# Kernel optimization log

Measured on AMD Instinct MI355X. Metric: run time of the kernel, lower is better.

Reference implementation:

```python
import jax, jax.numpy as jnp
import numpy as np

N_NODES = 100000
N_EDGES = 1600000
D = 64
L = 4
D_TGT = 32


def setup_inputs() -> dict:
    key = jax.random.key(0)
    ks = jax.random.split(key, 8)
    x = jax.random.normal(ks[0], (N_NODES, D), dtype=jnp.float32)
    edge_index = jax.random.randint(ks[1], (2, N_EDGES), 0, N_NODES, dtype=jnp.int64)
    s = 1.0 / np.sqrt(D)
    Wl = jax.random.normal(ks[2], (L, D, D), dtype=jnp.float32) * s
    bl = jnp.zeros((L, D), dtype=jnp.float32)
    Wr = jax.random.normal(ks[3], (L, D, D), dtype=jnp.float32) * s
    Wp = jax.random.normal(ks[4], (L * D, D_TGT), dtype=jnp.float32) * (1.0 / np.sqrt(L * D))
    bp = jnp.zeros((D_TGT,), dtype=jnp.float32)
    return {"x": x, "edge_index": edge_index, "Wl": Wl, "bl": bl, "Wr": Wr, "Wp": Wp, "bp": bp}


def reference(x, edge_index, Wl, bl, Wr, Wp, bp):
    src, dst = edge_index[0], edge_index[1]
    n = x.shape[0]
    # in-degree per node, clamped to avoid div-by-zero (PyG mean gives 0 for isolated nodes;
    # sum is 0 there so clamping matches)
    deg = jax.ops.segment_sum(jnp.ones_like(dst, dtype=x.dtype), dst, num_segments=n)
    deg = jnp.maximum(deg, 1.0)[:, None]
    h = x
    outs = []
    for i in range(Wl.shape[0]):
        # SAGEConv: out = lin_l(mean_{j in N(i)} h_j) + lin_r(h_i)
        agg = jax.ops.segment_sum(h[src], dst, num_segments=n) / deg
        h = agg @ Wl[i] + bl[i] + h @ Wr[i]
        outs.append(h)
    h_cat = jnp.concatenate(outs, axis=1)  # [N, L*D]
    return h_cat @ Wp + bp  # [N, D_TGT]
```

## Files before the change

### kernel.cpp

```cpp
#include <hip/hip_runtime.h>
#include <hip/hip_fp16.h>

#define NN 100000
#define NE 1600000
#define NNP (NN + 64)

#define NPB 512
#define NBUK ((NN + NPB - 1) / NPB)
#define EPB 2048
#define ABLK ((NE + EPB - 1) / EPB)
#define BCAP 10240

typedef _Float16 half8 __attribute__((ext_vector_type(8)));
typedef float f32x4 __attribute__((ext_vector_type(4)));


__global__ __launch_bounds__(256) void bucket_init(int* __restrict__ bucket_cur) {
  int t = blockIdx.x * 256 + threadIdx.x;
  if (t < NBUK) bucket_cur[t] = t * BCAP;
}

__global__ __launch_bounds__(256) void binA(const int* __restrict__ src,
                                            const int* __restrict__ dst,
                                            int* __restrict__ bucket_cur,
                                            uint2* __restrict__ binned) {
  __shared__ int hist[NBUK];
  __shared__ int sc[256];
  __shared__ int lbase[NBUK];
  __shared__ int gbase[NBUK];
  __shared__ int lcur[NBUK];
  __shared__ uint2 stage[EPB];
  int t = threadIdx.x;
  int e0 = blockIdx.x * EPB;
  if (t < NBUK) hist[t] = 0;
  __syncthreads();
  int es[8], ed[8];
#pragma unroll
  for (int j = 0; j < 8; ++j) {
    int e = e0 + t + j * 256;
    if (e < NE) {
      es[j] = src[e];
      ed[j] = dst[e];
      atomicAdd(&hist[ed[j] >> 9], 1);
    } else {
      es[j] = -1;
      ed[j] = 0;
    }
  }
  __syncthreads();
  sc[t] = (t < NBUK) ? hist[t] : 0;
  __syncthreads();
  for (int off = 1; off < 256; off <<= 1) {
    int v = (t >= off) ? sc[t - off] : 0;
    __syncthreads();
    sc[t] += v;
    __syncthreads();
  }
  if (t < NBUK) {
    int h = hist[t];
    int lb = sc[t] - h;
    lbase[t] = lb;
    lcur[t] = lb;
    if (h > 0) gbase[t] = atomicAdd(&bucket_cur[t], h);
  }
  __syncthreads();
#pragma unroll
  for (int j = 0; j < 8; ++j) {
    if (es[j] >= 0) {
      int b = ed[j] >> 9;
      int slot = atomicAdd(&lcur[b], 1);
      stage[slot] = make_uint2((unsigned)es[j], (unsigned)ed[j]);
    }
  }
  __syncthreads();
  int total = min(EPB, NE - e0);
  for (int i = t; i < total; i += 256) {
    uint2 p = stage[i];
    int b = (int)(p.y >> 9);
    binned[(size_t)gbase[b] + (i - lbase[b])] = p;
  }
}

__global__ __launch_bounds__(256) void bucket_scan(const int* __restrict__ bucket_cur,
                                                   int* __restrict__ bucket_base,
                                                   int* __restrict__ row_ptr) {
  __shared__ int part[256];
  int t = threadIdx.x;
  int v = (t < NBUK) ? (bucket_cur[t] - t * BCAP) : 0;
  part[t] = v;
  __syncthreads();
  for (int off = 1; off < 256; off <<= 1) {
    int u = (t >= off) ? part[t - off] : 0;
    __syncthreads();
    part[t] += u;
    __syncthreads();
  }
  if (t < NBUK) bucket_base[t] = part[t] - v;
  if (t == 0) row_ptr[NN] = NE;
}

__global__ __launch_bounds__(256) void binB(const uint2* __restrict__ binned,
                                            const int* __restrict__ bucket_cur,
                                            const int* __restrict__ bucket_base,
                                            int* __restrict__ row_ptr,
                                            float* __restrict__ deg_inv,
                                            int* __restrict__ col) {
  __shared__ int hist[NPB];
  __shared__ int cur2[NPB];
  __shared__ int part[256];
  __shared__ int srcS[BCAP];
  int b = blockIdx.x;
  int n0 = b * NPB;
  int n1 = min(n0 + NPB, NN);
  int cnt = bucket_cur[b] - b * BCAP;
  int gb = bucket_base[b];
  size_t seg = (size_t)b * BCAP;
  int t = threadIdx.x;
  hist[t] = 0;
  hist[t + 256] = 0;
  __syncthreads();
  for (int i = t; i < cnt; i += 256)
    atomicAdd(&hist[(int)binned[seg + i].y - n0], 1);
  __syncthreads();
  int c0 = hist[2 * t], c1 = hist[2 * t + 1];
  int s = c0 + c1;
  part[t] = s;
  __syncthreads();
  for (int off = 1; off < 256; off <<= 1) {
    int u = (t >= off) ? part[t - off] : 0;
    __syncthreads();
    part[t] += u;
    __syncthreads();
  }
  int excl = part[t] - s;
  cur2[2 * t] = excl;
  cur2[2 * t + 1] = excl + c0;
  int n = n0 + 2 * t;
  if (n < n1) {
    row_ptr[n] = gb + excl;
    deg_inv[n] = 1.0f / (float)(c0 > 1 ? c0 : 1);
  }
  if (n + 1 < n1) {
    row_ptr[n + 1] = gb + excl + c0;
    deg_inv[n + 1] = 1.0f / (float)(c1 > 1 ? c1 : 1);
  }
  __syncthreads();
  for (int i = t; i < cnt; i += 256) {
    uint2 p = binned[seg + i];
    int slot = atomicAdd(&cur2[(int)p.y - n0], 1);
    srcS[slot] = (int)p.x;
  }
  __syncthreads();
  for (int i = t; i < cnt; i += 256) col[(size_t)gb + i] = srcS[i];
}


__global__ __launch_bounds__(256) void tohalf(const float* __restrict__ x,
                                              __half* __restrict__ x16) {
  size_t o = ((size_t)blockIdx.x * 256 + threadIdx.x) * 8;
  float4 a = *(const float4*)(x + o);
  float4 b = *(const float4*)(x + o + 4);
  union { uint4 u; __half h[8]; } U;
  U.h[0] = __float2half(a.x); U.h[1] = __float2half(a.y);
  U.h[2] = __float2half(a.z); U.h[3] = __float2half(a.w);
  U.h[4] = __float2half(b.x); U.h[5] = __float2half(b.y);
  U.h[6] = __float2half(b.z); U.h[7] = __float2half(b.w);
  *(uint4*)(x16 + o) = U.u;
}


__global__ __launch_bounds__(256) void prep_weights(const float* __restrict__ Wl,
                                                    const float* __restrict__ Wr,
                                                    const float* __restrict__ Wp,
                                                    _Float16* __restrict__ WcatT,
                                                    _Float16* __restrict__ WpT) {
  int t = blockIdx.x * 256 + threadIdx.x;
  if (t < 4 * 64 * 128) {
    int l = t >> 13, rem = t & 8191, j = rem >> 7, k = rem & 127;
    float v = (k < 64) ? Wl[l * 4096 + k * 64 + j] : Wr[l * 4096 + (k - 64) * 64 + j];
    WcatT[t] = (_Float16)v;
  }
  if (t < 4 * 32 * 64) {
    int l = t >> 11, rem = t & 2047, j = rem >> 6, k = rem & 63;
    WpT[t] = (_Float16)Wp[(size_t)(l * 64 + k) * 32 + j];
  }
}


__global__ __launch_bounds__(256) void agg_kernel(const __half* __restrict__ h16,
                                                  const int* __restrict__ row_ptr,
                                                  const int* __restrict__ col,
                                                  const float* __restrict__ deg_inv,
                                                  __half* __restrict__ agg16) {
  int w = (int)((blockIdx.x * 256u + threadIdx.x) >> 6);
  int lane = threadIdx.x & 63;
  if (w >= NN) return;
  int beg = row_ptr[w], end = row_ptr[w + 1];
  float acc = 0.f;
  int e = beg;
  while (e < end) {
    int chunk = end - e;
    if (chunk > 64) chunk = 64;
    int cv = col[e + (lane < chunk ? lane : chunk - 1)];
    int i = 0;
    for (; i + 8 <= chunk; i += 8) {
      int s0 = __shfl(cv, i + 0, 64), s1 = __shfl(cv, i + 1, 64);
      int s2 = __shfl(cv, i + 2, 64), s3 = __shfl(cv, i + 3, 64);
      int s4 = __shfl(cv, i + 4, 64), s5 = __shfl(cv, i + 5, 64);
      int s6 = __shfl(cv, i + 6, 64), s7 = __shfl(cv, i + 7, 64);
      float v0 = __half2float(h16[(size_t)s0 * 64 + lane]);
      float v1 = __half2float(h16[(size_t)s1 * 64 + lane]);
      float v2 = __half2float(h16[(size_t)s2 * 64 + lane]);
      float v3 = __half2float(h16[(size_t)s3 * 64 + lane]);
      float v4 = __half2float(h16[(size_t)s4 * 64 + lane]);
      float v5 = __half2float(h16[(size_t)s5 * 64 + lane]);
      float v6 = __half2float(h16[(size_t)s6 * 64 + lane]);
      float v7 = __half2float(h16[(size_t)s7 * 64 + lane]);
      acc += ((v0 + v1) + (v2 + v3)) + ((v4 + v5) + (v6 + v7));
    }
    for (; i < chunk; ++i) {
      int s = __shfl(cv, i, 64);
      acc += __half2float(h16[(size_t)s * 64 + lane]);
    }
    e += chunk;
  }
  agg16[(size_t)w * 64 + lane] = __float2half(acc * deg_inv[w]);
}


#define PADC 72

__global__ __launch_bounds__(256) void layer_mfma(
    const _Float16* __restrict__ agg16, const _Float16* __restrict__ h16,
    const _Float16* __restrict__ WcatT, const float* __restrict__ bl,
    const _Float16* __restrict__ WpT, const float* __restrict__ bp,
    _Float16* __restrict__ hn16, float* __restrict__ out, int flags) {
  __shared__ _Float16 cS[64 * PADC];
  int tid = threadIdx.x;
  int w = tid >> 6, l = tid & 63;
  int lr = l & 15, lg = l >> 4;
  int base = blockIdx.x * 64;
  int arow = base + (w << 4) + lr;

  f32x4 acc[4];
#pragma unroll
  for (int ct = 0; ct < 4; ++ct) {
    float b = bl[ct * 16 + lr];
    acc[ct] = (f32x4){b, b, b, b};
  }
  const half8 a0 = *(const half8*)(agg16 + (size_t)arow * 64 + lg * 8);
  const half8 a1 = *(const half8*)(agg16 + (size_t)arow * 64 + 32 + lg * 8);
  const half8 a2 = *(const half8*)(h16 + (size_t)arow * 64 + lg * 8);
  const half8 a3 = *(const half8*)(h16 + (size_t)arow * 64 + 32 + lg * 8);
#pragma unroll
  for (int ct = 0; ct < 4; ++ct) {
    const _Float16* wb = WcatT + (ct * 16 + lr) * 128 + lg * 8;
    half8 b0 = *(const half8*)(wb);
    half8 b1 = *(const half8*)(wb + 32);
    half8 b2 = *(const half8*)(wb + 64);
    half8 b3 = *(const half8*)(wb + 96);
    acc[ct] = __builtin_amdgcn_mfma_f32_16x16x32_f16(a0, b0, acc[ct], 0, 0, 0);
    acc[ct] = __builtin_amdgcn_mfma_f32_16x16x32_f16(a1, b1, acc[ct], 0, 0, 0);
    acc[ct] = __builtin_amdgcn_mfma_f32_16x16x32_f16(a2, b2, acc[ct], 0, 0, 0);
    acc[ct] = __builtin_amdgcn_mfma_f32_16x16x32_f16(a3, b3, acc[ct], 0, 0, 0);
  }

#pragma unroll
  for (int ct = 0; ct < 4; ++ct)
#pragma unroll
    for (int r = 0; r < 4; ++r)
      cS[((w << 4) + (lg << 2) + r) * PADC + ct * 16 + lr] = (_Float16)acc[ct][r];
  __syncthreads();

  if (flags & 2) {
#pragma unroll
    for (int j = 0; j < 2; ++j) {
      int idx = tid + j * 256;
      int row = idx >> 3, c8 = (idx & 7) * 8;
      *(half8*)(hn16 + (size_t)(base + row) * 64 + c8) =
          *(const half8*)(cS + row * PADC + c8);
    }
  }

  f32x4 pacc[2];
#pragma unroll
  for (int pt = 0; pt < 2; ++pt) {
    int colo = pt * 16 + lr;
    if (flags & 1) {
      float b = bp[colo];
      pacc[pt] = (f32x4){b, b, b, b};
    } else {
#pragma unroll
      for (int r = 0; r < 4; ++r) {
        int row = base + (w << 4) + (lg << 2) + r;
        pacc[pt][r] = (row < NN) ? out[(size_t)row * 32 + colo] : 0.f;
      }
    }
  }
  const _Float16* crow = cS + ((w << 4) + lr) * PADC + lg * 8;
  half8 c0 = *(const half8*)(crow);
  half8 c1 = *(const half8*)(crow + 32);
#pragma unroll
  for (int pt = 0; pt < 2; ++pt) {
    const _Float16* wp = WpT + (pt * 16 + lr) * 64 + lg * 8;
    half8 w0 = *(const half8*)(wp);
    half8 w1 = *(const half8*)(wp + 32);
    pacc[pt] = __builtin_amdgcn_mfma_f32_16x16x32_f16(c0, w0, pacc[pt], 0, 0, 0);
    pacc[pt] = __builtin_amdgcn_mfma_f32_16x16x32_f16(c1, w1, pacc[pt], 0, 0, 0);
  }
#pragma unroll
  for (int pt = 0; pt < 2; ++pt) {
    int colo = pt * 16 + lr;
#pragma unroll
    for (int r = 0; r < 4; ++r) {
      int row = base + (w << 4) + (lg << 2) + r;
      if (row < NN) out[(size_t)row * 32 + colo] = pacc[pt][r];
    }
  }
}


extern "C" void kernel_launch(void* const* d_in, const int* in_sizes, int n_in,
                              void* d_out, int out_size, void* d_ws, size_t ws_size,
                              hipStream_t stream) {
  const float* x  = (const float*)d_in[0];
  const int*   ei = (const int*)d_in[1];
  const float* Wl = (const float*)d_in[2];
  const float* bl = (const float*)d_in[3];
  const float* Wr = (const float*)d_in[4];
  const float* Wp = (const float*)d_in[5];
  const float* bp = (const float*)d_in[6];
  float* out = (float*)d_out;

  char* ws = (char*)d_ws;
  size_t off = 0;
  auto alloc = [&](size_t bytes) {
    void* p = ws + off;
    off = (off + bytes + 255) & ~(size_t)255;
    return p;
  };
  int*      row_ptr     = (int*)alloc(((size_t)NN + 1) * 4);
  float*    deginv      = (float*)alloc((size_t)NN * 4);
  int*      col         = (int*)alloc((size_t)NE * 4);
  int*      bucket_cur  = (int*)alloc((size_t)NBUK * 4);
  int*      bucket_base = (int*)alloc((size_t)NBUK * 4);
  uint2*    binned      = (uint2*)alloc((size_t)NBUK * BCAP * 8);
  __half*   agg16       = (__half*)alloc((size_t)NNP * 64 * 2);
  __half*   x16         = (__half*)alloc((size_t)NNP * 64 * 2);
  __half*   h16A        = (__half*)alloc((size_t)NNP * 64 * 2);
  __half*   h16B        = (__half*)alloc((size_t)NNP * 64 * 2);
  _Float16* WcatT       = (_Float16*)alloc((size_t)4 * 64 * 128 * 2);
  _Float16* WpT         = (_Float16*)alloc((size_t)4 * 32 * 64 * 2);

  tohalf<<<3125, 256, 0, stream>>>(x, x16);
  prep_weights<<<128, 256, 0, stream>>>(Wl, Wr, Wp, WcatT, WpT);
  bucket_init<<<1, 256, 0, stream>>>(bucket_cur);
  binA<<<ABLK, 256, 0, stream>>>(ei, ei + NE, bucket_cur, binned);
  bucket_scan<<<1, 256, 0, stream>>>(bucket_cur, bucket_base, row_ptr);
  binB<<<NBUK, 256, 0, stream>>>(binned, bucket_cur, bucket_base, row_ptr, deginv, col);

  const __half* cur16 = x16;
  __half* bufs[2] = {h16A, h16B};
  int nblk = (NN + 63) / 64;
  for (int l = 0; l < 4; ++l) {
    agg_kernel<<<(NN + 3) / 4, 256, 0, stream>>>(cur16, row_ptr, col, deginv, agg16);
    __half* nxt = bufs[l & 1];
    int flags = (l == 0 ? 1 : 0) | (l < 3 ? 2 : 0);
    layer_mfma<<<nblk, 256, 0, stream>>>(
        (const _Float16*)agg16, (const _Float16*)cur16,
        WcatT + l * 8192, bl + l * 64, WpT + l * 2048, bp,
        (_Float16*)nxt, out, flags);
    cur16 = nxt;
  }
}
```

Baseline: 433.3 us.

## Fuse neighbor aggregation into per-layer MFMA kernel and pack binned edges

Folds the per-layer mean aggregation into the MFMA layer kernel. Each 64-node block gathers its neighbor sums into shared memory, then runs the dense transform on them, which removes the agg16 round trip through global memory and one launch per layer. Binned edge pairs are packed into a single 32-bit word (source shifted by 9, local destination in the low 9 bits), halving the binning traffic. The cost is fewer waves in flight for the latency-bound gather: each wave now walks 16 nodes serially in a block of 1563 instead of 25000 small blocks, so load imbalance and latency hiding could get worse.

```diff
diff --git a/kernel.cpp b/kernel.cpp
--- a/kernel.cpp
+++ b/kernel.cpp
@@ -23,7 +23,7 @@
 __global__ __launch_bounds__(256) void binA(const int* __restrict__ src,
                                             const int* __restrict__ dst,
                                             int* __restrict__ bucket_cur,
-                                            uint2* __restrict__ binned) {
+                                            unsigned* __restrict__ binned) {
   __shared__ int hist[NBUK];
   __shared__ int sc[256];
   __shared__ int lbase[NBUK];
@@ -77,7 +77,7 @@
   for (int i = t; i < total; i += 256) {
     uint2 p = stage[i];
     int b = (int)(p.y >> 9);
-    binned[(size_t)gbase[b] + (i - lbase[b])] = p;
+    binned[(size_t)gbase[b] + (i - lbase[b])] = (p.x << 9) | (p.y & 511u);
   }
 }
 
@@ -99,7 +99,7 @@
   if (t == 0) row_ptr[NN] = NE;
 }
 
-__global__ __launch_bounds__(256) void binB(const uint2* __restrict__ binned,
+__global__ __launch_bounds__(256) void binB(const unsigned* __restrict__ binned,
                                             const int* __restrict__ bucket_cur,
                                             const int* __restrict__ bucket_base,
                                             int* __restrict__ row_ptr,
@@ -120,7 +120,7 @@
   hist[t + 256] = 0;
   __syncthreads();
   for (int i = t; i < cnt; i += 256)
-    atomicAdd(&hist[(int)binned[seg + i].y - n0], 1);
+    atomicAdd(&hist[(int)(binned[seg + i] & 511u)], 1);
   __syncthreads();
   int c0 = hist[2 * t], c1 = hist[2 * t + 1];
   int s = c0 + c1;
@@ -146,9 +146,9 @@
   }
   __syncthreads();
   for (int i = t; i < cnt; i += 256) {
-    uint2 p = binned[seg + i];
-    int slot = atomicAdd(&cur2[(int)p.y - n0], 1);
-    srcS[slot] = (int)p.x;
+    unsigned p = binned[seg + i];
+    int slot = atomicAdd(&cur2[(int)(p & 511u)], 1);
+    srcS[slot] = (int)(p >> 9);
   }
   __syncthreads();
   for (int i = t; i < cnt; i += 256) col[(size_t)gb + i] = srcS[i];
@@ -187,69 +187,71 @@
 }
 
 
-__global__ __launch_bounds__(256) void agg_kernel(const __half* __restrict__ h16,
-                                                  const int* __restrict__ row_ptr,
-                                                  const int* __restrict__ col,
-                                                  const float* __restrict__ deg_inv,
-                                                  __half* __restrict__ agg16) {
-  int w = (int)((blockIdx.x * 256u + threadIdx.x) >> 6);
-  int lane = threadIdx.x & 63;
-  if (w >= NN) return;
-  int beg = row_ptr[w], end = row_ptr[w + 1];
-  float acc = 0.f;
-  int e = beg;
-  while (e < end) {
-    int chunk = end - e;
-    if (chunk > 64) chunk = 64;
-    int cv = col[e + (lane < chunk ? lane : chunk - 1)];
-    int i = 0;
-    for (; i + 8 <= chunk; i += 8) {
-      int s0 = __shfl(cv, i + 0, 64), s1 = __shfl(cv, i + 1, 64);
-      int s2 = __shfl(cv, i + 2, 64), s3 = __shfl(cv, i + 3, 64);
-      int s4 = __shfl(cv, i + 4, 64), s5 = __shfl(cv, i + 5, 64);
-      int s6 = __shfl(cv, i + 6, 64), s7 = __shfl(cv, i + 7, 64);
-      float v0 = __half2float(h16[(size_t)s0 * 64 + lane]);
-      float v1 = __half2float(h16[(size_t)s1 * 64 + lane]);
-      float v2 = __half2float(h16[(size_t)s2 * 64 + lane]);
-      float v3 = __half2float(h16[(size_t)s3 * 64 + lane]);
-      float v4 = __half2float(h16[(size_t)s4 * 64 + lane]);
-      float v5 = __half2float(h16[(size_t)s5 * 64 + lane]);
-      float v6 = __half2float(h16[(size_t)s6 * 64 + lane]);
-      float v7 = __half2float(h16[(size_t)s7 * 64 + lane]);
-      acc += ((v0 + v1) + (v2 + v3)) + ((v4 + v5) + (v6 + v7));
-    }
-    for (; i < chunk; ++i) {
-      int s = __shfl(cv, i, 64);
-      acc += __half2float(h16[(size_t)s * 64 + lane]);
-    }
-    e += chunk;
-  }
-  agg16[(size_t)w * 64 + lane] = __float2half(acc * deg_inv[w]);
-}
-
-
+#define PADA 72
 #define PADC 72
 
-__global__ __launch_bounds__(256) void layer_mfma(
-    const _Float16* __restrict__ agg16, const _Float16* __restrict__ h16,
+__global__ __launch_bounds__(256, 4) void fused_layer(
+    const _Float16* __restrict__ h16,
+    const int* __restrict__ row_ptr, const int* __restrict__ col,
+    const float* __restrict__ deginv,
     const _Float16* __restrict__ WcatT, const float* __restrict__ bl,
     const _Float16* __restrict__ WpT, const float* __restrict__ bp,
     _Float16* __restrict__ hn16, float* __restrict__ out, int flags) {
+  __shared__ _Float16 aggS[64 * PADA];
   __shared__ _Float16 cS[64 * PADC];
   int tid = threadIdx.x;
   int w = tid >> 6, l = tid & 63;
+  int base = blockIdx.x * 64;
+
+  for (int i = 0; i < 16; ++i) {
+    int n = base + (w << 4) + i;
+    float acc = 0.f;
+    if (n < NN) {
+      int beg = row_ptr[n], end = row_ptr[n + 1];
+      int e = beg;
+      while (e < end) {
+        int chunk = end - e;
+        if (chunk > 64) chunk = 64;
+        int cv = col[e + (l < chunk ? l : chunk - 1)];
+        int q = 0;
+        for (; q + 8 <= chunk; q += 8) {
+          int s0 = __shfl(cv, q + 0, 64), s1 = __shfl(cv, q + 1, 64);
+          int s2 = __shfl(cv, q + 2, 64), s3 = __shfl(cv, q + 3, 64);
+          int s4 = __shfl(cv, q + 4, 64), s5 = __shfl(cv, q + 5, 64);
+          int s6 = __shfl(cv, q + 6, 64), s7 = __shfl(cv, q + 7, 64);
+          float v0 = (float)h16[(size_t)s0 * 64 + l];
+          float v1 = (float)h16[(size_t)s1 * 64 + l];
+          float v2 = (float)h16[(size_t)s2 * 64 + l];
+          float v3 = (float)h16[(size_t)s3 * 64 + l];
+          float v4 = (float)h16[(size_t)s4 * 64 + l];
+          float v5 = (float)h16[(size_t)s5 * 64 + l];
+          float v6 = (float)h16[(size_t)s6 * 64 + l];
+          float v7 = (float)h16[(size_t)s7 * 64 + l];
+          acc += ((v0 + v1) + (v2 + v3)) + ((v4 + v5) + (v6 + v7));
+        }
+        for (; q < chunk; ++q) {
+          int s = __shfl(cv, q, 64);
+          acc += (float)h16[(size_t)s * 64 + l];
+        }
+        e += chunk;
+      }
+      acc *= deginv[n];
+    }
+    aggS[((w << 4) + i) * PADA + l] = (_Float16)acc;
+  }
+  __syncthreads();
+
   int lr = l & 15, lg = l >> 4;
-  int base = blockIdx.x * 64;
   int arow = base + (w << 4) + lr;
 
-  f32x4 acc[4];
+  f32x4 acc4[4];
 #pragma unroll
   for (int ct = 0; ct < 4; ++ct) {
     float b = bl[ct * 16 + lr];
-    acc[ct] = (f32x4){b, b, b, b};
-  }
-  const half8 a0 = *(const half8*)(agg16 + (size_t)arow * 64 + lg * 8);
-  const half8 a1 = *(const half8*)(agg16 + (size_t)arow * 64 + 32 + lg * 8);
+    acc4[ct] = (f32x4){b, b, b, b};
+  }
+  const half8 a0 = *(const half8*)(aggS + ((w << 4) + lr) * PADA + lg * 8);
+  const half8 a1 = *(const half8*)(aggS + ((w << 4) + lr) * PADA + 32 + lg * 8);
   const half8 a2 = *(const half8*)(h16 + (size_t)arow * 64 + lg * 8);
   const half8 a3 = *(const half8*)(h16 + (size_t)arow * 64 + 32 + lg * 8);
 #pragma unroll
@@ -259,17 +261,17 @@
     half8 b1 = *(const half8*)(wb + 32);
     half8 b2 = *(const half8*)(wb + 64);
     half8 b3 = *(const half8*)(wb + 96);
-    acc[ct] = __builtin_amdgcn_mfma_f32_16x16x32_f16(a0, b0, acc[ct], 0, 0, 0);
-    acc[ct] = __builtin_amdgcn_mfma_f32_16x16x32_f16(a1, b1, acc[ct], 0, 0, 0);
-    acc[ct] = __builtin_amdgcn_mfma_f32_16x16x32_f16(a2, b2, acc[ct], 0, 0, 0);
-    acc[ct] = __builtin_amdgcn_mfma_f32_16x16x32_f16(a3, b3, acc[ct], 0, 0, 0);
+    acc4[ct] = __builtin_amdgcn_mfma_f32_16x16x32_f16(a0, b0, acc4[ct], 0, 0, 0);
+    acc4[ct] = __builtin_amdgcn_mfma_f32_16x16x32_f16(a1, b1, acc4[ct], 0, 0, 0);
+    acc4[ct] = __builtin_amdgcn_mfma_f32_16x16x32_f16(a2, b2, acc4[ct], 0, 0, 0);
+    acc4[ct] = __builtin_amdgcn_mfma_f32_16x16x32_f16(a3, b3, acc4[ct], 0, 0, 0);
   }
 
 #pragma unroll
   for (int ct = 0; ct < 4; ++ct)
 #pragma unroll
     for (int r = 0; r < 4; ++r)
-      cS[((w << 4) + (lg << 2) + r) * PADC + ct * 16 + lr] = (_Float16)acc[ct][r];
+      cS[((w << 4) + (lg << 2) + r) * PADC + ct * 16 + lr] = (_Float16)acc4[ct][r];
   __syncthreads();
 
   if (flags & 2) {
@@ -344,8 +346,7 @@
   int*      col         = (int*)alloc((size_t)NE * 4);
   int*      bucket_cur  = (int*)alloc((size_t)NBUK * 4);
   int*      bucket_base = (int*)alloc((size_t)NBUK * 4);
-  uint2*    binned      = (uint2*)alloc((size_t)NBUK * BCAP * 8);
-  __half*   agg16       = (__half*)alloc((size_t)NNP * 64 * 2);
+  unsigned* binned      = (unsigned*)alloc((size_t)NBUK * BCAP * 4);
   __half*   x16         = (__half*)alloc((size_t)NNP * 64 * 2);
   __half*   h16A        = (__half*)alloc((size_t)NNP * 64 * 2);
   __half*   h16B        = (__half*)alloc((size_t)NNP * 64 * 2);
@@ -363,11 +364,10 @@
   __half* bufs[2] = {h16A, h16B};
   int nblk = (NN + 63) / 64;
   for (int l = 0; l < 4; ++l) {
-    agg_kernel<<<(NN + 3) / 4, 256, 0, stream>>>(cur16, row_ptr, col, deginv, agg16);
     __half* nxt = bufs[l & 1];
     int flags = (l == 0 ? 1 : 0) | (l < 3 ? 2 : 0);
-    layer_mfma<<<nblk, 256, 0, stream>>>(
-        (const _Float16*)agg16, (const _Float16*)cur16,
+    fused_layer<<<nblk, 256, 0, stream>>>(
+        (const _Float16*)cur16, row_ptr, col, deginv,
         WcatT + l * 8192, bl + l * 64, WpT + l * 2048, bp,
         (_Float16*)nxt, out, flags);
     cur16 = nxt;
```

New measurement: 419.2 us. -3.3%, faster.
